# Performance work log

Measured on AMD Instinct MI355X. Metric: run time of the kernel, lower is better.

Reference implementation:

```python
import jax, jax.numpy as jnp
import numpy as np

C_M = 256
C = 32
N_HEAD = 8
N_SEQ = 256
N_RES = 384


def setup_inputs() -> dict:
    key = jax.random.key(0)
    ks = jax.random.split(key, 10)
    s = 1.0 / np.sqrt(C_M)
    so = 1.0 / np.sqrt(N_HEAD * C)
    return {
        "m": jax.random.normal(ks[0], (N_SEQ, N_RES, C_M), dtype=jnp.float32),
        "ln_gamma": jnp.ones((C_M,), jnp.float32),
        "ln_beta": jnp.zeros((C_M,), jnp.float32),
        "Wq": jax.random.normal(ks[1], (C_M, N_HEAD * C), jnp.float32) * s,
        "Wk": jax.random.normal(ks[2], (C_M, N_HEAD * C), jnp.float32) * s,
        "Wv": jax.random.normal(ks[3], (C_M, N_HEAD * C), jnp.float32) * s,
        "Wg": jax.random.normal(ks[4], (C_M, N_HEAD * C), jnp.float32) * s,
        "bg": jnp.zeros((N_HEAD * C,), jnp.float32),
        "Wo": jax.random.normal(ks[5], (N_HEAD * C, C_M), jnp.float32) * so,
        "bo": jnp.zeros((C_M,), jnp.float32),
    }


def reference(m, ln_gamma, ln_beta, Wq, Wk, Wv, Wg, bg, Wo, bo):
    # LayerNorm over c_m
    mu = jnp.mean(m, axis=-1, keepdims=True)
    var = jnp.mean(jnp.square(m - mu), axis=-1, keepdims=True)
    x = (m - mu) * jax.lax.rsqrt(var + 1e-5) * ln_gamma + ln_beta

    # attention over N_seq axis (attn_dim=-3): move it next to features
    xt = jnp.swapaxes(x, 0, 1)  # (R, S, c_m)
    R, S = xt.shape[0], xt.shape[1]

    def heads(t):  # (R, S, H*c) -> (R, H, S, c)
        return jnp.swapaxes(t.reshape(R, S, N_HEAD, C), 1, 2)

    q = heads(xt @ Wq)
    k = heads(xt @ Wk)
    v = heads(xt @ Wv)

    logits = jnp.einsum("rhqc,rhkc->rhqk", q, k) / jnp.sqrt(jnp.asarray(C, x.dtype))
    attn = jax.nn.softmax(logits, axis=-1)
    o = jnp.einsum("rhqk,rhkc->rhqc", attn, v)  # (R, H, S, c)
    o = jnp.swapaxes(o, 1, 2).reshape(R, S, N_HEAD * C)

    g = jax.nn.sigmoid(xt @ Wg + bg)  # (R, S, H*c)
    out = (g * o) @ Wo + bo  # (R, S, c_m)
    return jnp.swapaxes(out, 0, 1)  # back to (S, R, c_m)
```

## Files before the change

### kernel.cpp

```cpp
#include <hip/hip_runtime.h>
#include <hip/hip_bf16.h>

#define NSEQ 256
#define NRES 384
#define CM   256
#define NH   8
#define HC   32

typedef __bf16 bf16x8_t __attribute__((ext_vector_type(8)));
typedef __bf16 bf16x4_t __attribute__((ext_vector_type(4)));
typedef float  f32x4_t  __attribute__((ext_vector_type(4)));

static __device__ __forceinline__ f32x4_t mfma16(bf16x8_t a, bf16x8_t b, f32x4_t c) {
    return __builtin_amdgcn_mfma_f32_16x16x32_bf16(a, b, c, 0, 0, 0);
}

static __device__ __forceinline__ bf16x4_t to_bf4(f32x4_t v) {
    bf16x4_t o;
    o[0] = (__bf16)v[0]; o[1] = (__bf16)v[1];
    o[2] = (__bf16)v[2]; o[3] = (__bf16)v[3];
    return o;
}

__global__ __launch_bounds__(256) void wprep_kernel(
        const float* __restrict__ wq, const float* __restrict__ wk,
        const float* __restrict__ wv, const float* __restrict__ wg,
        const float* __restrict__ wo, __bf16* __restrict__ wt) {
    __shared__ float tile[64][65];
    const float* src;
    switch (blockIdx.z) {
        case 0: src = wq; break; case 1: src = wk; break;
        case 2: src = wv; break; case 3: src = wg; break;
        default: src = wo; break;
    }
    __bf16* dst = wt + (size_t)blockIdx.z * (CM * CM);
    int k0 = blockIdx.x * 64;
    int n0 = blockIdx.y * 64;
    int lane = threadIdx.x & 63, wv2 = threadIdx.x >> 6;
    #pragma unroll
    for (int i = 0; i < 16; ++i) {
        int kk = wv2 * 16 + i;
        tile[kk][lane] = src[(size_t)(k0 + kk) * CM + n0 + lane];
    }
    __syncthreads();
    #pragma unroll
    for (int i = 0; i < 16; ++i) {
        int nn = wv2 * 16 + i;
        dst[(size_t)(n0 + nn) * CM + k0 + lane] = (__bf16)tile[lane][nn];
    }
}

__global__ __launch_bounds__(256) void ln_kernel(
        const float* __restrict__ m, const float* __restrict__ gamma,
        const float* __restrict__ beta, __bf16* __restrict__ x) {
    int w = threadIdx.x >> 6, lane = threadIdx.x & 63;
    int row = blockIdx.x * 4 + w;
    const float4 mv = *reinterpret_cast<const float4*>(m + (size_t)row * CM + lane * 4);
    float s1 = mv.x + mv.y + mv.z + mv.w;
    float s2 = mv.x * mv.x + mv.y * mv.y + mv.z * mv.z + mv.w * mv.w;
    #pragma unroll
    for (int d = 1; d < 64; d <<= 1) {
        s1 += __shfl_xor(s1, d);
        s2 += __shfl_xor(s2, d);
    }
    float mu  = s1 * (1.0f / CM);
    float var = s2 * (1.0f / CM) - mu * mu;
    float rs  = rsqrtf(var + 1e-5f);
    const float4 gv = *reinterpret_cast<const float4*>(gamma + lane * 4);
    const float4 bv = *reinterpret_cast<const float4*>(beta + lane * 4);
    int s = row / NRES;
    int r = row - s * NRES;
    int drow = r * NSEQ + s;
    bf16x4_t o;
    o[0] = (__bf16)((mv.x - mu) * rs * gv.x + bv.x);
    o[1] = (__bf16)((mv.y - mu) * rs * gv.y + bv.y);
    o[2] = (__bf16)((mv.z - mu) * rs * gv.z + bv.z);
    o[3] = (__bf16)((mv.w - mu) * rs * gv.w + bv.w);
    *reinterpret_cast<bf16x4_t*>(x + (size_t)drow * CM + lane * 4) = o;
}

__global__ __launch_bounds__(256, 2) void attn_kernel(
        const __bf16* __restrict__ x, const __bf16* __restrict__ wt,
        const float* __restrict__ bg, __bf16* __restrict__ go) {
    const int KRW = 40;
    const int VRW = 264;

    __shared__ __align__(16) char smem[57856];
    __bf16* k_s  = reinterpret_cast<__bf16*>(smem);
    __bf16* q_s  = reinterpret_cast<__bf16*>(smem + 20480);
    __bf16* v_sT = reinterpret_cast<__bf16*>(smem + 40960);

    int tid = threadIdx.x;
    int w = tid >> 6, lane = tid & 63;
    int l15 = lane & 15, g4 = lane >> 4;

    int bid = blockIdx.x;
    int nid = (bid & 7) * 384 + (bid >> 3);
    int r = nid >> 3, h = nid & 7;

    const __bf16* xr = x + (size_t)r * NSEQ * CM;

    const f32x4_t zf = {0.0f, 0.0f, 0.0f, 0.0f};
    f32x4_t acc[4][4][2];
    #pragma unroll
    for (int wi = 0; wi < 4; ++wi)
        #pragma unroll
        for (int mt = 0; mt < 4; ++mt)
            #pragma unroll
            for (int ct = 0; ct < 2; ++ct) acc[wi][mt][ct] = zf;

    #pragma unroll
    for (int kb = 0; kb < 8; ++kb) {
        bf16x8_t a[4];
        #pragma unroll
        for (int mt = 0; mt < 4; ++mt)
            a[mt] = *reinterpret_cast<const bf16x8_t*>(
                xr + (w * 64 + mt * 16 + l15) * CM + kb * 32 + g4 * 8);
        #pragma unroll
        for (int wi = 0; wi < 4; ++wi) {
            const __bf16* wslice = wt + (size_t)wi * (CM * CM) + (h * HC) * CM;
            bf16x8_t b[2];
            #pragma unroll
            for (int ct = 0; ct < 2; ++ct)
                b[ct] = *reinterpret_cast<const bf16x8_t*>(
                    wslice + (ct * 16 + l15) * CM + kb * 32 + g4 * 8);
            if (wi < 2) {
                #pragma unroll
                for (int nt = 0; nt < 4; ++nt)
                    #pragma unroll
                    for (int cm = 0; cm < 2; ++cm)
                        acc[wi][nt][cm] = mfma16(b[cm], a[nt], acc[wi][nt][cm]);
            } else {
                #pragma unroll
                for (int mt = 0; mt < 4; ++mt)
                    #pragma unroll
                    for (int ct = 0; ct < 2; ++ct)
                        acc[wi][mt][ct] = mfma16(a[mt], b[ct], acc[wi][mt][ct]);
            }
        }
    }

    #pragma unroll
    for (int mt = 0; mt < 4; ++mt)
        #pragma unroll
        for (int ct = 0; ct < 2; ++ct) {
            int qrow = (w * 64 + mt * 16 + l15) * KRW + ct * 16 + g4 * 4;
            *reinterpret_cast<bf16x4_t*>(q_s + qrow) = to_bf4(acc[0][mt][ct]);
            *reinterpret_cast<bf16x4_t*>(k_s + qrow) = to_bf4(acc[1][mt][ct]);
            *reinterpret_cast<bf16x4_t*>(
                v_sT + (ct * 16 + l15) * VRW + w * 64 + mt * 16 + g4 * 4) =
                to_bf4(acc[2][mt][ct]);
        }
    __syncthreads();

    bf16x8_t kf[16];
    #pragma unroll
    for (int kt = 0; kt < 16; ++kt)
        kf[kt] = *reinterpret_cast<const bf16x8_t*>(k_s + (kt * 16 + l15) * KRW + g4 * 8);
    bf16x8_t qf[4];
    #pragma unroll
    for (int qt = 0; qt < 4; ++qt)
        qf[qt] = *reinterpret_cast<const bf16x8_t*>(q_s + (w * 64 + qt * 16 + l15) * KRW + g4 * 8);
    __syncthreads();

    __bf16* p_s = reinterpret_cast<__bf16*>(smem + w * 8448);

    float bgv[2];
    bgv[0] = bg[h * HC + l15];
    bgv[1] = bg[h * HC + 16 + l15];
    const float cs = 0.17677669529663687f * 1.4426950408889634f;
    const float l2e = 1.4426950408889634f;

    __bf16* gor = go + (((size_t)r * NH + h) * NSEQ) * HC;

    #pragma unroll
    for (int qt = 0; qt < 4; ++qt) {
        f32x4_t sacc[16];
        #pragma unroll
        for (int kt = 0; kt < 16; ++kt) sacc[kt] = zf;
        #pragma unroll
        for (int kt = 0; kt < 16; ++kt) sacc[kt] = mfma16(kf[kt], qf[qt], sacc[kt]);

        float s4[4] = {0.0f, 0.0f, 0.0f, 0.0f};
        #pragma unroll
        for (int kt = 0; kt < 16; ++kt)
            #pragma unroll
            for (int i = 0; i < 4; ++i) {
                float e = exp2f(sacc[kt][i] * cs);
                sacc[kt][i] = e;
                s4[i] += e;
            }
        float sum = (s4[0] + s4[1]) + (s4[2] + s4[3]);
        sum += __shfl_xor(sum, 16);
        sum += __shfl_xor(sum, 32);
        float inv = 1.0f / sum;

        #pragma unroll
        for (int kt = 0; kt < 16; ++kt) {
            bf16x4_t pv;
            #pragma unroll
            for (int i = 0; i < 4; ++i) pv[i] = (__bf16)(sacc[kt][i] * inv);
            *reinterpret_cast<bf16x4_t*>(p_s + l15 * VRW + kt * 16 + g4 * 4) = pv;
        }

        f32x4_t oacc[2];
        oacc[0] = zf; oacc[1] = zf;
        #pragma unroll
        for (int kb = 0; kb < 8; ++kb) {
            bf16x8_t pa = *reinterpret_cast<const bf16x8_t*>(p_s + l15 * VRW + kb * 32 + g4 * 8);
            #pragma unroll
            for (int ct = 0; ct < 2; ++ct) {
                bf16x8_t vb = *reinterpret_cast<const bf16x8_t*>(
                    v_sT + (ct * 16 + l15) * VRW + kb * 32 + g4 * 8);
                oacc[ct] = mfma16(pa, vb, oacc[ct]);
            }
        }

        #pragma unroll
        for (int ct = 0; ct < 2; ++ct)
            #pragma unroll
            for (int i = 0; i < 4; ++i) {
                float t  = acc[3][qt][ct][i] + bgv[ct];
                float gs = 1.0f / (1.0f + exp2f(-t * l2e));
                int srow = w * 64 + qt * 16 + g4 * 4 + i;
                gor[(size_t)srow * HC + ct * 16 + l15] = (__bf16)(gs * oacc[ct][i]);
            }
    }
}

__global__ __launch_bounds__(256, 2) void outgemm_kernel(
        const __bf16* __restrict__ go, const __bf16* __restrict__ wto,
        const float* __restrict__ bo, float* __restrict__ out) {
    int tid = threadIdx.x, w = tid >> 6, lane = tid & 63;
    int l15 = lane & 15, g4 = lane >> 4;
    int j0 = blockIdx.x * 64 + w * 16;
    int rb = j0 >> 8;
    int s0 = j0 & (NSEQ - 1);
    const __bf16* gor = go + ((size_t)rb * NH) * NSEQ * HC;
    const f32x4_t zf = {0.0f, 0.0f, 0.0f, 0.0f};
    f32x4_t acc[16];
    #pragma unroll
    for (int nt = 0; nt < 16; ++nt) acc[nt] = zf;
    #pragma unroll
    for (int kb = 0; kb < 8; ++kb) {
        bf16x8_t a = *reinterpret_cast<const bf16x8_t*>(
            gor + ((size_t)kb * NSEQ + s0 + l15) * HC + g4 * 8);
        #pragma unroll
        for (int nt = 0; nt < 16; ++nt) {
            bf16x8_t b = *reinterpret_cast<const bf16x8_t*>(
                wto + (nt * 16 + l15) * CM + kb * 32 + g4 * 8);
            acc[nt] = mfma16(a, b, acc[nt]);
        }
    }
    #pragma unroll
    for (int nt = 0; nt < 16; ++nt) {
        float bias = bo[nt * 16 + l15];
        #pragma unroll
        for (int i = 0; i < 4; ++i) {
            int s = s0 + g4 * 4 + i;
            out[((size_t)(s * NRES + rb)) * CM + nt * 16 + l15] = acc[nt][i] + bias;
        }
    }
}

extern "C" void kernel_launch(void* const* d_in, const int* in_sizes, int n_in,
                              void* d_out, int out_size, void* d_ws, size_t ws_size,
                              hipStream_t stream) {
    const float* m     = (const float*)d_in[0];
    const float* gamma = (const float*)d_in[1];
    const float* beta  = (const float*)d_in[2];
    const float* wq    = (const float*)d_in[3];
    const float* wk    = (const float*)d_in[4];
    const float* wv    = (const float*)d_in[5];
    const float* wg    = (const float*)d_in[6];
    const float* bg    = (const float*)d_in[7];
    const float* wo    = (const float*)d_in[8];
    const float* bo    = (const float*)d_in[9];

    char* ws = (char*)d_ws;
    const size_t X_OFF  = 1u << 20;
    const size_t GO_OFF = X_OFF + (size_t)NRES * NSEQ * CM * 2;
    const size_t NEED   = GO_OFF + (size_t)NRES * NSEQ * CM * 2;
    if (ws_size < NEED) return;

    __bf16* wt = (__bf16*)ws;
    __bf16* x  = (__bf16*)(ws + X_OFF);
    __bf16* go = (__bf16*)(ws + GO_OFF);

    wprep_kernel<<<dim3(4, 4, 5), 256, 0, stream>>>(wq, wk, wv, wg, wo, wt);
    ln_kernel<<<(NSEQ * NRES) / 4, 256, 0, stream>>>(m, gamma, beta, x);
    attn_kernel<<<NRES * NH, 256, 0, stream>>>(x, wt, bg, go);
    outgemm_kernel<<<(NRES * NSEQ) / 64, 256, 0, stream>>>(go, wt + 4 * (CM * CM), bo, (float*)d_out);
}
```

Measured before the change: 315.8 us.

## Cut attention LDS footprint to raise occupancy, build Q fragments via shuffles

Q fragments are no longer staged through shared memory. They are packed to bf16 in registers and rearranged into the MFMA operand layout with cross-lane shuffles. The P tile is written and consumed in two halves, so the per-wave P buffer shrinks. Together these cut shared memory from about 57KB to 37KB, which lets launch bounds allow 3 blocks per CU instead of 2. MFMA sections are also wrapped in s_setprio. The risks are register pressure under the tighter occupancy bound and the added shuffle/select cost per query tile.

```diff
diff --git a/kernel.cpp b/kernel.cpp
--- a/kernel.cpp
+++ b/kernel.cpp
@@ -10,6 +10,7 @@
 typedef __bf16 bf16x8_t __attribute__((ext_vector_type(8)));
 typedef __bf16 bf16x4_t __attribute__((ext_vector_type(4)));
 typedef float  f32x4_t  __attribute__((ext_vector_type(4)));
+typedef unsigned int u32x4_t __attribute__((ext_vector_type(4)));
 
 static __device__ __forceinline__ f32x4_t mfma16(bf16x8_t a, bf16x8_t b, f32x4_t c) {
     return __builtin_amdgcn_mfma_f32_16x16x32_bf16(a, b, c, 0, 0, 0);
@@ -20,6 +21,12 @@
     o[0] = (__bf16)v[0]; o[1] = (__bf16)v[1];
     o[2] = (__bf16)v[2]; o[3] = (__bf16)v[3];
     return o;
+}
+
+static __device__ __forceinline__ unsigned int pkbf(float a, float b) {
+    union { __bf16 h[2]; unsigned int u; } t;
+    t.h[0] = (__bf16)a; t.h[1] = (__bf16)b;
+    return t.u;
 }
 
 __global__ __launch_bounds__(256) void wprep_kernel(
@@ -79,16 +86,16 @@
     *reinterpret_cast<bf16x4_t*>(x + (size_t)drow * CM + lane * 4) = o;
 }
 
-__global__ __launch_bounds__(256, 2) void attn_kernel(
+__global__ __launch_bounds__(256, 3) void attn_kernel(
         const __bf16* __restrict__ x, const __bf16* __restrict__ wt,
         const float* __restrict__ bg, __bf16* __restrict__ go) {
     const int KRW = 40;
     const int VRW = 264;
-
-    __shared__ __align__(16) char smem[57856];
+    const int PRW = 136;
+
+    __shared__ __align__(16) char smem[37376];
     __bf16* k_s  = reinterpret_cast<__bf16*>(smem);
-    __bf16* q_s  = reinterpret_cast<__bf16*>(smem + 20480);
-    __bf16* v_sT = reinterpret_cast<__bf16*>(smem + 40960);
+    __bf16* v_sT = reinterpret_cast<__bf16*>(smem + 20480);
 
     int tid = threadIdx.x;
     int w = tid >> 6, lane = tid & 63;
@@ -140,13 +147,22 @@
         }
     }
 
+    unsigned int qpk[4][2][2];
+    #pragma unroll
+    for (int qt = 0; qt < 4; ++qt)
+        #pragma unroll
+        for (int cm = 0; cm < 2; ++cm) {
+            qpk[qt][cm][0] = pkbf(acc[0][qt][cm][0], acc[0][qt][cm][1]);
+            qpk[qt][cm][1] = pkbf(acc[0][qt][cm][2], acc[0][qt][cm][3]);
+        }
+
     #pragma unroll
     for (int mt = 0; mt < 4; ++mt)
         #pragma unroll
         for (int ct = 0; ct < 2; ++ct) {
-            int qrow = (w * 64 + mt * 16 + l15) * KRW + ct * 16 + g4 * 4;
-            *reinterpret_cast<bf16x4_t*>(q_s + qrow) = to_bf4(acc[0][mt][ct]);
-            *reinterpret_cast<bf16x4_t*>(k_s + qrow) = to_bf4(acc[1][mt][ct]);
+            *reinterpret_cast<bf16x4_t*>(
+                k_s + (w * 64 + mt * 16 + l15) * KRW + ct * 16 + g4 * 4) =
+                to_bf4(acc[1][mt][ct]);
             *reinterpret_cast<bf16x4_t*>(
                 v_sT + (ct * 16 + l15) * VRW + w * 64 + mt * 16 + g4 * 4) =
                 to_bf4(acc[2][mt][ct]);
@@ -157,13 +173,9 @@
     #pragma unroll
     for (int kt = 0; kt < 16; ++kt)
         kf[kt] = *reinterpret_cast<const bf16x8_t*>(k_s + (kt * 16 + l15) * KRW + g4 * 8);
-    bf16x8_t qf[4];
-    #pragma unroll
-    for (int qt = 0; qt < 4; ++qt)
-        qf[qt] = *reinterpret_cast<const bf16x8_t*>(q_s + (w * 64 + qt * 16 + l15) * KRW + g4 * 8);
     __syncthreads();
 
-    __bf16* p_s = reinterpret_cast<__bf16*>(smem + w * 8448);
+    __bf16* p_s = reinterpret_cast<__bf16*>(smem + w * 4352);
 
     float bgv[2];
     bgv[0] = bg[h * HC + l15];
@@ -171,15 +183,38 @@
     const float cs = 0.17677669529663687f * 1.4426950408889634f;
     const float l2e = 1.4426950408889634f;
 
+    int src0 = l15 + 16 * ((2 * g4) & 3);
+    int src1 = l15 + 16 * ((2 * g4 + 1) & 3);
+    int cmsel = g4 >> 1;
+
     __bf16* gor = go + (((size_t)r * NH + h) * NSEQ) * HC;
 
     #pragma unroll
     for (int qt = 0; qt < 4; ++qt) {
+        u32x4_t qw;
+        {
+            unsigned int a0 = __shfl((int)qpk[qt][0][0], src0);
+            unsigned int a1 = __shfl((int)qpk[qt][0][1], src0);
+            unsigned int b0 = __shfl((int)qpk[qt][1][0], src0);
+            unsigned int b1 = __shfl((int)qpk[qt][1][1], src0);
+            unsigned int c0 = __shfl((int)qpk[qt][0][0], src1);
+            unsigned int c1 = __shfl((int)qpk[qt][0][1], src1);
+            unsigned int d0 = __shfl((int)qpk[qt][1][0], src1);
+            unsigned int d1 = __shfl((int)qpk[qt][1][1], src1);
+            qw[0] = cmsel ? b0 : a0;
+            qw[1] = cmsel ? b1 : a1;
+            qw[2] = cmsel ? d0 : c0;
+            qw[3] = cmsel ? d1 : c1;
+        }
+        bf16x8_t qfr = __builtin_bit_cast(bf16x8_t, qw);
+
         f32x4_t sacc[16];
         #pragma unroll
         for (int kt = 0; kt < 16; ++kt) sacc[kt] = zf;
-        #pragma unroll
-        for (int kt = 0; kt < 16; ++kt) sacc[kt] = mfma16(kf[kt], qf[qt], sacc[kt]);
+        __builtin_amdgcn_s_setprio(1);
+        #pragma unroll
+        for (int kt = 0; kt < 16; ++kt) sacc[kt] = mfma16(kf[kt], qfr, sacc[kt]);
+        __builtin_amdgcn_s_setprio(0);
 
         float s4[4] = {0.0f, 0.0f, 0.0f, 0.0f};
         #pragma unroll
@@ -195,25 +230,30 @@
         sum += __shfl_xor(sum, 32);
         float inv = 1.0f / sum;
 
-        #pragma unroll
-        for (int kt = 0; kt < 16; ++kt) {
-            bf16x4_t pv;
-            #pragma unroll
-            for (int i = 0; i < 4; ++i) pv[i] = (__bf16)(sacc[kt][i] * inv);
-            *reinterpret_cast<bf16x4_t*>(p_s + l15 * VRW + kt * 16 + g4 * 4) = pv;
-        }
-
         f32x4_t oacc[2];
         oacc[0] = zf; oacc[1] = zf;
         #pragma unroll
-        for (int kb = 0; kb < 8; ++kb) {
-            bf16x8_t pa = *reinterpret_cast<const bf16x8_t*>(p_s + l15 * VRW + kb * 32 + g4 * 8);
-            #pragma unroll
-            for (int ct = 0; ct < 2; ++ct) {
-                bf16x8_t vb = *reinterpret_cast<const bf16x8_t*>(
-                    v_sT + (ct * 16 + l15) * VRW + kb * 32 + g4 * 8);
-                oacc[ct] = mfma16(pa, vb, oacc[ct]);
-            }
+        for (int hk = 0; hk < 2; ++hk) {
+            #pragma unroll
+            for (int k2 = 0; k2 < 8; ++k2) {
+                bf16x4_t pv;
+                #pragma unroll
+                for (int i = 0; i < 4; ++i) pv[i] = (__bf16)(sacc[hk * 8 + k2][i] * inv);
+                *reinterpret_cast<bf16x4_t*>(p_s + l15 * PRW + k2 * 16 + g4 * 4) = pv;
+            }
+            __builtin_amdgcn_s_setprio(1);
+            #pragma unroll
+            for (int kb2 = 0; kb2 < 4; ++kb2) {
+                bf16x8_t pa = *reinterpret_cast<const bf16x8_t*>(
+                    p_s + l15 * PRW + kb2 * 32 + g4 * 8);
+                #pragma unroll
+                for (int ct = 0; ct < 2; ++ct) {
+                    bf16x8_t vb = *reinterpret_cast<const bf16x8_t*>(
+                        v_sT + (ct * 16 + l15) * VRW + hk * 128 + kb2 * 32 + g4 * 8);
+                    oacc[ct] = mfma16(pa, vb, oacc[ct]);
+                }
+            }
+            __builtin_amdgcn_s_setprio(0);
         }
 
         #pragma unroll
```

Measured after the change: 453.7 us. +43.7%, slower.
